# Optimization experiments

Hardware: AMD Instinct MI355X
Metric: run time of the kernel (lower is better)

## Reference

```python
import jax, jax.numpy as jnp
import numpy as np
import math

B, L, D, H = 4, 2048, 1024, 16
DK = D // H

def setup_inputs() -> dict:
    key = jax.random.key(0)
    ks = jax.random.split(key, 12)
    inp = {
        'query': jax.random.normal(ks[0], (B, L, D), dtype=jnp.float32),
        'key':   jax.random.normal(ks[1], (B, L, D), dtype=jnp.float32),
        'value': jax.random.normal(ks[2], (B, L, D), dtype=jnp.float32),
        # causal mask, broadcast over batch: [B, L, L], 1 = keep, 0 = masked
        'mask': jnp.broadcast_to(jnp.tril(jnp.ones((L, L), dtype=jnp.int32)), (B, L, L)),
    }
    s = 1.0 / math.sqrt(D)
    inp['Wq'] = jax.random.uniform(ks[3], (D, D), jnp.float32, -s, s)
    inp['bq'] = jax.random.uniform(ks[4], (D,), jnp.float32, -s, s)
    inp['Wk'] = jax.random.uniform(ks[5], (D, D), jnp.float32, -s, s)
    inp['bk'] = jax.random.uniform(ks[6], (D,), jnp.float32, -s, s)
    inp['Wv'] = jax.random.uniform(ks[7], (D, D), jnp.float32, -s, s)
    inp['bv'] = jax.random.uniform(ks[8], (D,), jnp.float32, -s, s)
    inp['Wo'] = jax.random.uniform(ks[9], (D, D), jnp.float32, -s, s)
    inp['bo'] = jax.random.uniform(ks[10], (D,), jnp.float32, -s, s)
    return inp

def reference(query, key, value, mask, Wq, bq, Wk, bk, Wv, bv, Wo, bo):
    # projections (torch Linear: x @ W.T + b), split heads: [B, H, L, DK]
    def proj(x, W, b):
        return (x @ W.T + b).reshape(B, -1, H, DK).transpose(0, 2, 1, 3)
    q = proj(query, Wq, bq)
    k = proj(key, Wk, bk)
    v = proj(value, Wv, bv)
    scores = jnp.einsum('bhqd,bhkd->bhqk', q, k) / math.sqrt(DK)
    scores = jnp.where(mask[:, None, :, :] == 0, jnp.float32(-1e9), scores)
    p_attn = jax.nn.softmax(scores, axis=-1)  # dropout p=0.0 -> identity
    x = jnp.einsum('bhqk,bhkd->bhqd', p_attn, v)
    x = x.transpose(0, 2, 1, 3).reshape(B, -1, D)
    return x @ Wo.T + bo
```

## Files before the change

kernel.cpp:

```cpp
#include <hip/hip_runtime.h>
#include <hip/hip_bf16.h>

#define B_ 4
#define H_ 16
#define L_ 2048
#define D_ 1024
#define DK_ 64

typedef __attribute__((ext_vector_type(8))) __bf16 bf16x8;
typedef __attribute__((ext_vector_type(4))) __bf16 bf16x4;
typedef __attribute__((ext_vector_type(4))) float f32x4;

#define MFMA16(a, b, c) __builtin_amdgcn_mfma_f32_16x16x32_bf16(a, b, c, 0, 0, 0)

typedef const __attribute__((address_space(1))) void gv_t;
typedef __attribute__((address_space(3))) void lv_t;

template<int NI>
__device__ __forceinline__ void stage_swz(const __bf16* __restrict__ g,
                                          size_t gstride, __bf16* lds, int t)
{
    const int wave = t >> 6;
#pragma unroll
    for (int i = 0; i < NI; ++i) {
        const int row = i * 32 + (t >> 3);
        const int s   = (t & 7) ^ (row & 7);
        __builtin_amdgcn_global_load_lds(
            (gv_t*)(g + (size_t)row * gstride + s * 8),
            (lv_t*)(lds + (size_t)(i * 32 + wave * 8) * 64),
            16, 0, 0);
    }
}

__device__ __forceinline__ bf16x8 lds_frag(const __bf16* base, int row, int kbyte)
{
    const char* p = (const char*)base + row * 128 + (kbyte ^ ((row & 7) << 4));
    return *(const bf16x8*)p;
}

struct CastArgs {
    const float* s[7];
    __bf16*      d[7];
    int          n[7];
};

__global__ __launch_bounds__(256)
void cast_all(CastArgs a)
{
    const int seg = blockIdx.y;
    const int n   = a.n[seg];
    const float* __restrict__ s = a.s[seg];
    __bf16* __restrict__ d = a.d[seg];
    for (int i = (blockIdx.x * 256 + threadIdx.x) * 8; i < n; i += gridDim.x * 256 * 8) {
        float4 f0 = *reinterpret_cast<const float4*>(&s[i]);
        float4 f1 = *reinterpret_cast<const float4*>(&s[i + 4]);
        bf16x8 v;
        v[0] = (__bf16)f0.x; v[1] = (__bf16)f0.y; v[2] = (__bf16)f0.z; v[3] = (__bf16)f0.w;
        v[4] = (__bf16)f1.x; v[5] = (__bf16)f1.y; v[6] = (__bf16)f1.z; v[7] = (__bf16)f1.w;
        *reinterpret_cast<bf16x8*>(&d[i]) = v;
    }
}

struct QKVDst {
    const float* bq; const float* bk; const float* bvv;
    __bf16* qh; __bf16* kh; __bf16* vt;
};

#define ASEG ((size_t)B_ * L_ * D_)

template<int MODE>
__global__ __launch_bounds__(256, 4)
void gemm_bf16(const __bf16* __restrict__ A, const __bf16* __restrict__ W,
               const float* __restrict__ bias, void* __restrict__ Cout,
               int M, int N, int K, QKVDst qd)
{
    constexpr int BM = 128, BN = 64, BK = 64;
    __shared__ __bf16 As[BM * BK];
    __shared__ __bf16 Bs[BN * BK];

    const int t = threadIdx.x;
    const int wave = t >> 6, lane = t & 63;
    const int g4 = lane >> 4, l16 = lane & 15;
    const int wr = wave >> 1, wc = wave & 1;
    const int fid = blockIdx.x;
    const int idx = fid >> 3;
    const int m0 = (((fid & 7) << 3) + (idx & 7)) * BM;
    const int n0 = (idx >> 3) * BN;
    const int which = (MODE == 3) ? (n0 >> 10) : 0;
    if (MODE == 3) A += (size_t)which * ASEG;

    f32x4 acc[4][2];
#pragma unroll
    for (int m = 0; m < 4; ++m)
#pragma unroll
        for (int n = 0; n < 2; ++n) acc[m][n] = {0.f, 0.f, 0.f, 0.f};

    for (int kt = 0; kt < K; kt += BK) {
        __syncthreads();
        stage_swz<4>(A + (size_t)m0 * K + kt, (size_t)K, As, t);
        stage_swz<2>(W + (size_t)n0 * K + kt, (size_t)K, Bs, t);
        __syncthreads();
#pragma unroll
        for (int kk = 0; kk < 2; ++kk) {
            bf16x8 af[4], bfr[2];
#pragma unroll
            for (int m = 0; m < 4; ++m)
                af[m] = lds_frag(As, wr * 64 + m * 16 + l16, kk * 64 + g4 * 16);
#pragma unroll
            for (int n = 0; n < 2; ++n)
                bfr[n] = lds_frag(Bs, wc * 32 + n * 16 + l16, kk * 64 + g4 * 16);
#pragma unroll
            for (int m = 0; m < 4; ++m)
#pragma unroll
                for (int n = 0; n < 2; ++n)
                    acc[m][n] = MFMA16(af[m], bfr[n], acc[m][n]);
        }
    }

#pragma unroll
    for (int n = 0; n < 2; ++n) {
        const int gc = n0 + wc * 32 + n * 16 + l16;
        float bval;
        int dd = gc, hh = 0, dk = 0;
        if (MODE == 3) {
            dd = gc & 1023; hh = dd >> 6; dk = dd & 63;
            const float* bp = (which == 0) ? qd.bq : (which == 1) ? qd.bk : qd.bvv;
            bval = bp[dd];
        } else {
            bval = bias[gc];
        }
#pragma unroll
        for (int m = 0; m < 4; ++m) {
            const int gr0 = m0 + wr * 64 + m * 16 + g4 * 4;
            if (MODE == 3) {
                const int bb = gr0 >> 11, l0 = gr0 & (L_ - 1);
                if (which < 2) {
                    __bf16* dst = (which == 0) ? qd.qh : qd.kh;
#pragma unroll
                    for (int r = 0; r < 4; ++r)
                        dst[(((size_t)(bb * H_ + hh)) * L_ + l0 + r) * DK_ + dk] =
                            (__bf16)(acc[m][n][r] + bval);
                } else {
                    bf16x4 v;
#pragma unroll
                    for (int r = 0; r < 4; ++r) v[r] = (__bf16)(acc[m][n][r] + bval);
                    *reinterpret_cast<bf16x4*>(
                        &qd.vt[(((size_t)(bb * H_ + hh)) * DK_ + dk) * L_ + l0]) = v;
                }
            } else {
#pragma unroll
                for (int r = 0; r < 4; ++r)
                    ((float*)Cout)[(size_t)(gr0 + r) * N + gc] = acc[m][n][r] + bval;
            }
        }
    }
}

#define SCALE2 0.18033688011112042f
#define THR    6.0f

__global__ __launch_bounds__(256, 4)
void attn_mfma(const __bf16* __restrict__ Qh, const __bf16* __restrict__ Kh,
               const __bf16* __restrict__ Vt, __bf16* __restrict__ Xb)
{
    __shared__ __bf16 Ks[2][64 * 64];
    __shared__ __bf16 Vs[2][64 * 64];
    __shared__ __bf16 Ps[64 * 64];

    const int t = threadIdx.x;
    const int wave = t >> 6, lane = t & 63;
    const int g4 = lane >> 4, l16 = lane & 15;
    const int fid   = blockIdx.x;
    const int xcd   = fid & 7;
    const int idx   = fid >> 3;
    const int strip = 31 - (idx >> 3);
    const int hb_id = xcd * 8 + (idx & 7);
    const int h = hb_id & 15, b = hb_id >> 4;
    const int qb = strip * 64;
    const size_t hb = (size_t)(b * H_ + h) * L_ * DK_;
    const __bf16* Qp = Qh + hb;
    const __bf16* Kp = Kh + hb;
    const __bf16* Vp = Vt + hb;
    const int qrow0 = qb + wave * 16;

    bf16x8 qf[2];
#pragma unroll
    for (int kk = 0; kk < 2; ++kk)
        qf[kk] = *reinterpret_cast<const bf16x8*>(
            &Qp[(size_t)(qrow0 + l16) * DK_ + kk * 32 + g4 * 8]);

    f32x4 O[4];
#pragma unroll
    for (int n = 0; n < 4; ++n) O[n] = {0.f, 0.f, 0.f, 0.f};
    float m_run = -1e30f, l_run = 0.f;

    const int ntile = strip + 1;
    stage_swz<2>(Kp, DK_, Ks[0], t);
    stage_swz<2>(Vp, L_, Vs[0], t);
    __syncthreads();

    int cur = 0;
    for (int it = 0; it < ntile; ++it) {
        if (it + 1 < ntile) {
            stage_swz<2>(Kp + (size_t)(it + 1) * 64 * DK_, DK_, Ks[cur ^ 1], t);
            stage_swz<2>(Vp + (it + 1) * 64, L_, Vs[cur ^ 1], t);
        }
        const int kv0 = it * 64;

        f32x4 st[4];
#pragma unroll
        for (int n = 0; n < 4; ++n) st[n] = {0.f, 0.f, 0.f, 0.f};
        __builtin_amdgcn_s_setprio(1);
#pragma unroll
        for (int kk = 0; kk < 2; ++kk) {
            bf16x8 kf[4];
#pragma unroll
            for (int n = 0; n < 4; ++n)
                kf[n] = lds_frag(Ks[cur], n * 16 + l16, kk * 64 + g4 * 16);
#pragma unroll
            for (int n = 0; n < 4; ++n)
                st[n] = MFMA16(kf[n], qf[kk], st[n]);
        }
        __builtin_amdgcn_s_setprio(0);

        if (it == strip) {
            const int qg = qrow0 + l16;
#pragma unroll
            for (int n = 0; n < 4; ++n)
#pragma unroll
                for (int r = 0; r < 4; ++r)
                    if (kv0 + n * 16 + g4 * 4 + r > qg) st[n][r] = -1e30f;
        }

        float mx = st[0][0];
#pragma unroll
        for (int n = 0; n < 4; ++n)
#pragma unroll
            for (int r = 0; r < 4; ++r)
                if (n + r) mx = fmaxf(mx, st[n][r]);
        mx = fmaxf(mx, __shfl_xor(mx, 16));
        mx = fmaxf(mx, __shfl_xor(mx, 32));
        const float mxs = mx * SCALE2;

        const bool grow = !__all(mxs - m_run <= THR);
        float al = 1.f;
        if (grow) {
            const float mn = fmaxf(m_run, mxs);
            al = exp2f(m_run - mn);
            m_run = mn;
        }

        char* Pw = (char*)Ps + (wave * 16 + l16) * 128;
        float lb = 0.f;
#pragma unroll
        for (int n = 0; n < 4; ++n) {
            bf16x4 pv;
#pragma unroll
            for (int r = 0; r < 4; ++r) {
                const float p = exp2f(fmaf(st[n][r], SCALE2, -m_run));
                lb += p;
                pv[r] = (__bf16)p;
            }
            *(bf16x4*)(Pw + ((n * 32 + g4 * 8) ^ ((l16 & 7) << 4))) = pv;
        }
        lb += __shfl_xor(lb, 16);
        lb += __shfl_xor(lb, 32);
        l_run = al * l_run + lb;

        if (grow) {
#pragma unroll
            for (int r = 0; r < 4; ++r) {
                const float alr = __shfl(al, g4 * 4 + r);
#pragma unroll
                for (int n = 0; n < 4; ++n) O[n][r] *= alr;
            }
        }

        const __bf16* Pr = Ps + wave * 16 * 64;
        __builtin_amdgcn_s_setprio(1);
#pragma unroll
        for (int kk = 0; kk < 2; ++kk) {
            bf16x8 pa = lds_frag(Pr, l16, kk * 64 + g4 * 16);
            bf16x8 vf[4];
#pragma unroll
            for (int n = 0; n < 4; ++n)
                vf[n] = lds_frag(Vs[cur], n * 16 + l16, kk * 64 + g4 * 16);
#pragma unroll
            for (int n = 0; n < 4; ++n)
                O[n] = MFMA16(pa, vf[n], O[n]);
        }
        __builtin_amdgcn_s_setprio(0);

        __syncthreads();
        cur ^= 1;
    }

    const float rl = 1.0f / l_run;
#pragma unroll
    for (int r = 0; r < 4; ++r) {
        const float inv = __shfl(rl, g4 * 4 + r);
        const int qrow = qrow0 + g4 * 4 + r;
#pragma unroll
        for (int n = 0; n < 4; ++n)
            Xb[((size_t)b * L_ + qrow) * D_ + h * DK_ + n * 16 + l16] =
                (__bf16)(O[n][r] * inv);
    }
}

extern "C" void kernel_launch(void* const* d_in, const int* in_sizes, int n_in,
                              void* d_out, int out_size, void* d_ws, size_t ws_size,
                              hipStream_t stream)
{
    (void)in_sizes; (void)n_in; (void)out_size; (void)ws_size;
    const float* query = (const float*)d_in[0];
    const float* key   = (const float*)d_in[1];
    const float* value = (const float*)d_in[2];
    const float* Wq = (const float*)d_in[4];
    const float* bq = (const float*)d_in[5];
    const float* Wk = (const float*)d_in[6];
    const float* bk = (const float*)d_in[7];
    const float* Wv = (const float*)d_in[8];
    const float* bv = (const float*)d_in[9];
    const float* Wo = (const float*)d_in[10];
    const float* bo = (const float*)d_in[11];

    const size_t SZ = (size_t)B_ * L_ * D_;
    const size_t WSZ = (size_t)D_ * D_;
    __bf16* wsb = (__bf16*)d_ws;
    __bf16* qb_ = wsb;
    __bf16* Qh  = wsb + 3 * SZ;
    __bf16* Kh  = wsb + 4 * SZ;
    __bf16* Vt  = wsb + 5 * SZ;
    __bf16* Xb  = wsb + 6 * SZ;
    __bf16* Wqkv = wsb + 7 * SZ;
    __bf16* Wob  = Wqkv + 3 * WSZ;

    CastArgs ca;
    ca.s[0] = query; ca.s[1] = key; ca.s[2] = value;
    ca.s[3] = Wq; ca.s[4] = Wk; ca.s[5] = Wv; ca.s[6] = Wo;
    ca.d[0] = qb_; ca.d[1] = qb_ + SZ; ca.d[2] = qb_ + 2 * SZ;
    ca.d[3] = Wqkv; ca.d[4] = Wqkv + WSZ; ca.d[5] = Wqkv + 2 * WSZ; ca.d[6] = Wob;
    ca.n[0] = ca.n[1] = ca.n[2] = (int)SZ;
    ca.n[3] = ca.n[4] = ca.n[5] = ca.n[6] = (int)WSZ;
    cast_all<<<dim3(1024, 7), 256, 0, stream>>>(ca);

    QKVDst qd;
    qd.bq = bq; qd.bk = bk; qd.bvv = bv;
    qd.qh = Qh; qd.kh = Kh; qd.vt = Vt;

    const int M = B_ * L_;
    gemm_bf16<3><<<64 * 48, 256, 0, stream>>>(qb_, Wqkv, nullptr, nullptr,
                                              M, 3 * D_, D_, qd);
    attn_mfma<<<32 * H_ * B_, 256, 0, stream>>>(Qh, Kh, Vt, Xb);
    gemm_bf16<2><<<64 * 16, 256, 0, stream>>>(Xb, Wob, bo, d_out, M, D_, D_, qd);
}
```

Measured before the change: 349.6 us.

## Use larger double-buffered 256x128 GEMM tiles with 512-thread blocks

Replaces the 128x64 single-buffered projection GEMM with a 256x128 tile computed by 8 waves, each owning a 64x64 sub-tile. The LDS buffers are double-buffered so the next K-slice loads while MFMAs run, which also drops one barrier per iteration. The aim is more operand reuse per loaded byte and overlap of global loads with compute. In exchange it uses more LDS and registers per block, launches fewer blocks, and remaps the XCD tile swizzle.

```diff
diff --git a/kernel.cpp b/kernel.cpp
--- a/kernel.cpp
+++ b/kernel.cpp
@@ -28,6 +28,22 @@
         __builtin_amdgcn_global_load_lds(
             (gv_t*)(g + (size_t)row * gstride + s * 8),
             (lv_t*)(lds + (size_t)(i * 32 + wave * 8) * 64),
+            16, 0, 0);
+    }
+}
+
+template<int NI>
+__device__ __forceinline__ void stage512(const __bf16* __restrict__ g,
+                                         size_t gstride, __bf16* lds, int t)
+{
+    const int wave = t >> 6;
+#pragma unroll
+    for (int i = 0; i < NI; ++i) {
+        const int row = i * 64 + (t >> 3);
+        const int s   = (t & 7) ^ (row & 7);
+        __builtin_amdgcn_global_load_lds(
+            (gv_t*)(g + (size_t)row * gstride + s * 8),
+            (lv_t*)(lds + (size_t)(i * 64 + wave * 8) * 64),
             16, 0, 0);
     }
 }
@@ -69,57 +85,65 @@
 #define ASEG ((size_t)B_ * L_ * D_)
 
 template<int MODE>
-__global__ __launch_bounds__(256, 4)
-void gemm_bf16(const __bf16* __restrict__ A, const __bf16* __restrict__ W,
-               const float* __restrict__ bias, void* __restrict__ Cout,
-               int M, int N, int K, QKVDst qd)
-{
-    constexpr int BM = 128, BN = 64, BK = 64;
-    __shared__ __bf16 As[BM * BK];
-    __shared__ __bf16 Bs[BN * BK];
+__global__ __launch_bounds__(512, 2)
+void gemm_big(const __bf16* __restrict__ A, const __bf16* __restrict__ W,
+              const float* __restrict__ bias, void* __restrict__ Cout,
+              int N, QKVDst qd)
+{
+    constexpr int BM = 256, BN = 128, BK = 64, K = 1024;
+    __shared__ __bf16 As[2][BM * BK];
+    __shared__ __bf16 Bs[2][BN * BK];
 
     const int t = threadIdx.x;
     const int wave = t >> 6, lane = t & 63;
     const int g4 = lane >> 4, l16 = lane & 15;
     const int wr = wave >> 1, wc = wave & 1;
     const int fid = blockIdx.x;
+    const int xcd = fid & 7;
     const int idx = fid >> 3;
-    const int m0 = (((fid & 7) << 3) + (idx & 7)) * BM;
-    const int n0 = (idx >> 3) * BN;
+    const int m0 = (xcd * 4 + (idx & 3)) * BM;
+    const int n0 = (idx >> 2) * BN;
     const int which = (MODE == 3) ? (n0 >> 10) : 0;
-    if (MODE == 3) A += (size_t)which * ASEG;
-
-    f32x4 acc[4][2];
+    const __bf16* Ap = (MODE == 3) ? A + (size_t)which * ASEG : A;
+
+    f32x4 acc[4][4];
 #pragma unroll
     for (int m = 0; m < 4; ++m)
 #pragma unroll
-        for (int n = 0; n < 2; ++n) acc[m][n] = {0.f, 0.f, 0.f, 0.f};
-
-    for (int kt = 0; kt < K; kt += BK) {
+        for (int n = 0; n < 4; ++n) acc[m][n] = {0.f, 0.f, 0.f, 0.f};
+
+    stage512<4>(Ap + (size_t)m0 * K, (size_t)K, As[0], t);
+    stage512<2>(W  + (size_t)n0 * K, (size_t)K, Bs[0], t);
+    __syncthreads();
+
+    int cur = 0;
+    for (int ti = 0; ti < K / BK; ++ti) {
+        if (ti + 1 < K / BK) {
+            stage512<4>(Ap + (size_t)m0 * K + (ti + 1) * BK, (size_t)K, As[cur ^ 1], t);
+            stage512<2>(W  + (size_t)n0 * K + (ti + 1) * BK, (size_t)K, Bs[cur ^ 1], t);
+        }
+#pragma unroll
+        for (int kk = 0; kk < 2; ++kk) {
+            bf16x8 af[4], bfr[4];
+#pragma unroll
+            for (int m = 0; m < 4; ++m)
+                af[m] = lds_frag(As[cur], wr * 64 + m * 16 + l16, kk * 64 + g4 * 16);
+#pragma unroll
+            for (int n = 0; n < 4; ++n)
+                bfr[n] = lds_frag(Bs[cur], wc * 64 + n * 16 + l16, kk * 64 + g4 * 16);
+#pragma unroll
+            for (int m = 0; m < 4; ++m)
+#pragma unroll
+                for (int n = 0; n < 4; ++n)
+                    acc[m][n] = MFMA16(af[m], bfr[n], acc[m][n]);
+        }
         __syncthreads();
-        stage_swz<4>(A + (size_t)m0 * K + kt, (size_t)K, As, t);
-        stage_swz<2>(W + (size_t)n0 * K + kt, (size_t)K, Bs, t);
-        __syncthreads();
-#pragma unroll
-        for (int kk = 0; kk < 2; ++kk) {
-            bf16x8 af[4], bfr[2];
-#pragma unroll
-            for (int m = 0; m < 4; ++m)
-                af[m] = lds_frag(As, wr * 64 + m * 16 + l16, kk * 64 + g4 * 16);
-#pragma unroll
-            for (int n = 0; n < 2; ++n)
-                bfr[n] = lds_frag(Bs, wc * 32 + n * 16 + l16, kk * 64 + g4 * 16);
-#pragma unroll
-            for (int m = 0; m < 4; ++m)
-#pragma unroll
-                for (int n = 0; n < 2; ++n)
-                    acc[m][n] = MFMA16(af[m], bfr[n], acc[m][n]);
-        }
-    }
-
-#pragma unroll
-    for (int n = 0; n < 2; ++n) {
-        const int gc = n0 + wc * 32 + n * 16 + l16;
+        cur ^= 1;
+    }
+
+#pragma unroll
+    for (int n = 0; n < 4; ++n) {
+        const int gc = n0 + wc * 64 + n * 16 + l16;
         float bval;
         int dd = gc, hh = 0, dk = 0;
         if (MODE == 3) {
@@ -348,9 +372,7 @@
     qd.bq = bq; qd.bk = bk; qd.bvv = bv;
     qd.qh = Qh; qd.kh = Kh; qd.vt = Vt;
 
-    const int M = B_ * L_;
-    gemm_bf16<3><<<64 * 48, 256, 0, stream>>>(qb_, Wqkv, nullptr, nullptr,
-                                              M, 3 * D_, D_, qd);
+    gemm_big<3><<<768, 512, 0, stream>>>(qb_, Wqkv, nullptr, nullptr, 3 * D_, qd);
     attn_mfma<<<32 * H_ * B_, 256, 0, stream>>>(Qh, Kh, Vt, Xb);
-    gemm_bf16<2><<<64 * 16, 256, 0, stream>>>(Xb, Wob, bo, d_out, M, D_, D_, qd);
-}
+    gemm_big<2><<<256, 512, 0, stream>>>(Xb, Wob, bo, d_out, D_, qd);
+}
```

Measured after the change: 369.7 us. 5.7% more time.
